# Optimization experiments

Hardware: AMD Instinct MI355X
Metric: run time of the kernel (lower is better)

## Reference

```python
import jax, jax.numpy as jnp
import numpy as np

B, S, H, D = 2, 2048, 16, 128

def setup_inputs() -> dict:
    key = jax.random.key(0)
    kq, kk, kv = jax.random.split(key, 3)
    query = jax.random.normal(kq, (B, S, H, D), dtype=jnp.float32)
    key_t = jax.random.normal(kk, (B, S, H, D), dtype=jnp.float32)
    value = jax.random.normal(kv, (B, S, H, D), dtype=jnp.float32)
    return {"query": query, "key": key_t, "value": value}

def reference(query, key, value):
    # Single-device equivalent: SeqAllToAll4D is identity (world_size=1),
    # ring flash attention == exact softmax attention.
    # Layout [B, S, H, D] (flash-attn convention), non-causal, no dropout.
    scale = 1.0 / jnp.sqrt(jnp.asarray(query.shape[-1], query.dtype))
    # scores: [B, H, Sq, Sk]
    scores = jnp.einsum("bqhd,bkhd->bhqk", query, key) * scale
    probs = jax.nn.softmax(scores, axis=-1)
    out = jnp.einsum("bhqk,bkhd->bqhd", probs, value)
    return out
```

## Files before the change

kernel.cpp:

```cpp
#include <hip/hip_runtime.h>
#include <hip/hip_bf16.h>

#define NB 2
#define NS 2048
#define NH 16
#define ND 128
#define SROW (NH*ND)

#define QBLK 128
#define KBLK 64
#define NTHR 256
#define NT   (NS/KBLK)


typedef __attribute__((ext_vector_type(4))) float f32x4;
typedef __attribute__((ext_vector_type(8))) __bf16 bf16x8;
typedef __attribute__((ext_vector_type(4))) __bf16 bf16x4;
typedef __attribute__((ext_vector_type(8))) short s16x8;
typedef __attribute__((ext_vector_type(4))) short s16x4;

#define AS1(p) ((const __attribute__((address_space(1))) void*)(p))
#define AS3(p) ((__attribute__((address_space(3))) void*)(p))

__device__ __forceinline__ short f2bf(float f) {
  union { float f; unsigned u; } v; v.f = f;
  unsigned r = v.u + 0x7fffu + ((v.u >> 16) & 1u);
  return (short)(r >> 16);
}

__global__ __launch_bounds__(256)
void prep_k2(const float* __restrict__ K, char* __restrict__ Kp) {
  const float sc = 0.08838834764831845f * 1.4426950408889634f;
  size_t i = (size_t)blockIdx.x * 256 + threadIdx.x;
  int g = (int)(i & 31);
  size_t row = i >> 5;
  int h = (int)(row & (NH - 1));
  size_t bs = row >> 4;
  int s = (int)(bs & (NS - 1));
  int b = (int)(bs >> 11);
  float4 x = *(const float4*)(K + row * ND + g * 4);
  bf16x4 w = { (__bf16)(x.x * sc), (__bf16)(x.y * sc), (__bf16)(x.z * sc), (__bf16)(x.w * sc) };
  int bh = b * NH + h;
  int kt = s >> 6, r = s & 63;
  int x8 = r * 256 + g * 8;
  int swz = x8 ^ ((r & 7) << 4);
  *(bf16x4*)(Kp + (((size_t)(bh * 32 + kt)) << 14) + swz) = w;
}

__global__ __launch_bounds__(256)
void prep_v2(const float* __restrict__ V, char* __restrict__ Vp) {
  __shared__ short tile[64 * 136];
  int gid = blockIdx.x;
  int kt = gid & 31;
  int bh = gid >> 5;
  int b = bh >> 4, h = bh & 15;
  int s0 = kt * 64;
  const float* src = V + ((size_t)b * NS * NH + h) * ND;
#pragma unroll
  for (int it = 0; it < 8; ++it) {
    int idx = threadIdx.x + it * 256;
    int r = idx >> 5;
    int c = (idx & 31) * 4;
    float4 x = *(const float4*)(src + (size_t)(s0 + r) * SROW + c);
    bf16x4 w = { (__bf16)x.x, (__bf16)x.y, (__bf16)x.z, (__bf16)x.w };
    *(bf16x4*)&tile[r * 136 + c] = w;
  }
  __syncthreads();
  char* dst = Vp + (((size_t)(bh * 32 + kt)) << 14);
#pragma unroll
  for (int it = 0; it < 8; ++it) {
    int id = threadIdx.x + it * 256;
    int d = id >> 4;
    int c = (id >> 1) & 7;
    int half = id & 1;
    int kvb = c * 8 + half * 4;
    s16x4 w = { tile[(kvb + 0) * 136 + d], tile[(kvb + 1) * 136 + d],
                tile[(kvb + 2) * 136 + d], tile[(kvb + 3) * 136 + d] };
    int vb0 = (c >> 2) * 64 + (((c & 3) * 2) & 3) * 16 + ((c & 3) >> 1) * 8;
    int x = d * 128 + vb0 + half * 16;
    int swz = x ^ ((d & 7) << 4);
    *(s16x4*)(dst + swz) = w;
  }
}

__global__ __launch_bounds__(NTHR, 2)
void attn_fwd13(const float* __restrict__ Q, const char* __restrict__ Kp,
                const char* __restrict__ Vp, float* __restrict__ O)
{
  __shared__ __align__(16) char klds[2 * 16384];
  __shared__ __align__(16) char vlds[2 * 16384];

  const int tid  = threadIdx.x;
  const int wave = tid >> 6;
  const int lane = tid & 63;
  const int g    = lane >> 4;
  const int lr   = lane & 15;

  const int L  = blockIdx.x;
  const int bh = (L & 7) + 8 * ((L >> 3) & 3);
  const int qb = L >> 5;
  const int b  = bh >> 4;
  const int h  = bh & 15;

  const float* Qb = Q + ((size_t)b * NS * NH + h) * ND;
  float*       Ob = O + ((size_t)b * NS * NH + h) * ND;
  const char*  kimg = Kp + ((size_t)bh << 19);
  const char*  vimg = Vp + ((size_t)bh << 19);

  const int wq0 = qb * QBLK + wave * 32;

  bf16x8 qf[2][4];
#pragma unroll
  for (int qt = 0; qt < 2; ++qt) {
    const float* qp = Qb + (size_t)(wq0 + qt * 16 + lr) * SROW;
#pragma unroll
    for (int kc = 0; kc < 4; ++kc) {
      const int d0 = kc * 32 + g * 8;
      float4 a = *(const float4*)(qp + d0);
      float4 c = *(const float4*)(qp + d0 + 4);
      bf16x8 f;
      f[0] = (__bf16)a.x; f[1] = (__bf16)a.y; f[2] = (__bf16)a.z; f[3] = (__bf16)a.w;
      f[4] = (__bf16)c.x; f[5] = (__bf16)c.y; f[6] = (__bf16)c.z; f[7] = (__bf16)c.w;
      qf[qt][kc] = f;
    }
  }

  f32x4 oacc[2][8];
#pragma unroll
  for (int qt = 0; qt < 2; ++qt)
#pragma unroll
    for (int dc = 0; dc < 8; ++dc) oacc[qt][dc] = (f32x4){0.f, 0.f, 0.f, 0.f};
  float lpart[2] = {0.f, 0.f};

  const int kmask = (lr & 7) << 4;
  int kca[4];
#pragma unroll
  for (int kc = 0; kc < 4; ++kc)
    kca[kc] = (lr * 256 + kc * 64 + g * 16) ^ kmask;
  const int vca0 = (lr * 128 + g * 16) ^ kmask;
  const int vca1 = (lr * 128 + 64 + g * 16) ^ kmask;

  const int stago = wave * 4096 + lane * 16;
  const int stagl = wave * 4096;

#define STAGE(PAR, KT)                                                         \
  {                                                                            \
    const char* kg = kimg + ((size_t)(KT) << 14) + stago;                      \
    const char* vg = vimg + ((size_t)(KT) << 14) + stago;                      \
    _Pragma("unroll")                                                          \
    for (int ii = 0; ii < 4; ++ii) {                                           \
      __builtin_amdgcn_global_load_lds(AS1(kg + ii * 1024),                    \
          AS3(klds + (PAR) * 16384 + stagl + ii * 1024), 16, 0, 0);            \
      __builtin_amdgcn_global_load_lds(AS1(vg + ii * 1024),                    \
          AS3(vlds + (PAR) * 16384 + stagl + ii * 1024), 16, 0, 0);            \
    }                                                                          \
  }

  STAGE(0, 0);
  __syncthreads();

#pragma unroll 2
  for (int kt = 0; kt < NT; ++kt) {
    const int po = (kt & 1) * 16384;

    if (kt + 1 < NT) STAGE((kt + 1) & 1, kt + 1);

    f32x4 sacc[2][4];
    __builtin_amdgcn_s_setprio(1);
#pragma unroll
    for (int nb = 0; nb < 4; ++nb) {
      f32x4 a0 = {0.f, 0.f, 0.f, 0.f};
      f32x4 a1 = {0.f, 0.f, 0.f, 0.f};
#pragma unroll
      for (int kc = 0; kc < 4; ++kc) {
        bf16x8 kf = *(const bf16x8*)(klds + po + nb * 4096 + kca[kc]);
        a0 = __builtin_amdgcn_mfma_f32_16x16x32_bf16(kf, qf[0][kc], a0, 0, 0, 0);
        a1 = __builtin_amdgcn_mfma_f32_16x16x32_bf16(kf, qf[1][kc], a1, 0, 0, 0);
      }
      sacc[0][nb] = a0;
      sacc[1][nb] = a1;
    }
    __builtin_amdgcn_s_setprio(0);

    bf16x8 pf[2][2];
#pragma unroll
    for (int qt = 0; qt < 2; ++qt) {
#pragma unroll
      for (int nb = 0; nb < 4; ++nb)
#pragma unroll
        for (int i = 0; i < 4; ++i) {
          float p = exp2f(sacc[qt][nb][i]);
          sacc[qt][nb][i] = p;
          lpart[qt] += p;
        }
      bf16x8 t0, t1;
#pragma unroll
      for (int i = 0; i < 4; ++i) {
        t0[i]     = (__bf16)sacc[qt][0][i];
        t0[i + 4] = (__bf16)sacc[qt][1][i];
        t1[i]     = (__bf16)sacc[qt][2][i];
        t1[i + 4] = (__bf16)sacc[qt][3][i];
      }
      pf[qt][0] = t0;
      pf[qt][1] = t1;
    }

    __builtin_amdgcn_s_setprio(1);
#pragma unroll
    for (int dc = 0; dc < 8; ++dc) {
      bf16x8 vf0 = *(const bf16x8*)(vlds + po + dc * 2048 + vca0);
      bf16x8 vf1 = *(const bf16x8*)(vlds + po + dc * 2048 + vca1);
      oacc[0][dc] = __builtin_amdgcn_mfma_f32_16x16x32_bf16(pf[0][0], vf0, oacc[0][dc], 0, 0, 0);
      oacc[1][dc] = __builtin_amdgcn_mfma_f32_16x16x32_bf16(pf[1][0], vf0, oacc[1][dc], 0, 0, 0);
      oacc[0][dc] = __builtin_amdgcn_mfma_f32_16x16x32_bf16(pf[0][1], vf1, oacc[0][dc], 0, 0, 0);
      oacc[1][dc] = __builtin_amdgcn_mfma_f32_16x16x32_bf16(pf[1][1], vf1, oacc[1][dc], 0, 0, 0);
    }
    __builtin_amdgcn_s_setprio(0);

    __syncthreads();
  }

#pragma unroll
  for (int qt = 0; qt < 2; ++qt) {
    float l = lpart[qt];
    l += __shfl_xor(l, 16);
    l += __shfl_xor(l, 32);
    float inv = 1.0f / l;
#pragma unroll
    for (int i = 0; i < 4; ++i) {
      float invm = __shfl(inv, g * 4 + i);
      float* orow = Ob + (size_t)(wq0 + qt * 16 + g * 4 + i) * SROW;
#pragma unroll
      for (int dc = 0; dc < 8; ++dc)
        orow[dc * 16 + lr] = oacc[qt][dc][i] * invm;
    }
  }
#undef STAGE
}

__global__ __launch_bounds__(256, 2)
void attn_fwd_legacy(const float* __restrict__ Q, const float* __restrict__ K,
                     const float* __restrict__ V, float* __restrict__ O)
{
  __shared__ __align__(16) short k_lds[64 * 136];
  __shared__ __align__(16) short vt_lds[ND * 72];
  __shared__ __align__(16) short p_lds[4 * 16 * 72];

  const int tid = threadIdx.x;
  const int wave = tid >> 6;
  const int lane = tid & 63;
  const int g = lane >> 4;
  const int lr = lane & 15;

  const int nqb = NS / 64;
  const int qb = blockIdx.x % nqb;
  const int bh = blockIdx.x / nqb;
  const int b = bh / NH;
  const int h = bh % NH;

  const float scale = 0.08838834764831845f * 1.4426950408889634f;
  const size_t base = ((size_t)b * NS * NH + h) * ND;
  const float* Qb = Q + base;
  const float* Kbp = K + base;
  const float* Vb = V + base;
  float* Ob = O + base;
  const int q0 = qb * 64 + wave * 16;

  bf16x8 qf[4];
  {
    const float* qp = Qb + (size_t)(q0 + lr) * SROW;
#pragma unroll
    for (int kc = 0; kc < 4; ++kc) {
      const int d0 = kc * 32 + g * 8;
      float4 a = *(const float4*)(qp + d0);
      float4 c = *(const float4*)(qp + d0 + 4);
      s16x8 f;
      f[0] = f2bf(a.x * scale); f[1] = f2bf(a.y * scale);
      f[2] = f2bf(a.z * scale); f[3] = f2bf(a.w * scale);
      f[4] = f2bf(c.x * scale); f[5] = f2bf(c.y * scale);
      f[6] = f2bf(c.z * scale); f[7] = f2bf(c.w * scale);
      qf[kc] = __builtin_bit_cast(bf16x8, f);
    }
  }

  f32x4 oacc[8];
#pragma unroll
  for (int dc = 0; dc < 8; ++dc) oacc[dc] = (f32x4){0.f, 0.f, 0.f, 0.f};
  float mrun[4] = {-1e30f, -1e30f, -1e30f, -1e30f};
  float lrun[4] = {0.f, 0.f, 0.f, 0.f};

  for (int kt = 0; kt < NS / 64; ++kt) {
    const int kv0 = kt * 64;
    __syncthreads();
#pragma unroll
    for (int it = 0; it < 8; ++it) {
      int idx = tid + it * 256;
      int r = idx >> 5;
      int c = (idx & 31) << 2;
      float4 x = *(const float4*)(Kbp + (size_t)(kv0 + r) * SROW + c);
      s16x4 w = { f2bf(x.x), f2bf(x.y), f2bf(x.z), f2bf(x.w) };
      *(s16x4*)&k_lds[r * 136 + c] = w;
    }
#pragma unroll
    for (int it = 0; it < 2; ++it) {
      int sub = tid + it * 256;
      int skv = (sub >> 5) << 2;
      int sd = (sub & 31) << 2;
      const float* vp = Vb + (size_t)(kv0 + skv) * SROW + sd;
      float4 r0 = *(const float4*)(vp);
      float4 r1 = *(const float4*)(vp + SROW);
      float4 r2 = *(const float4*)(vp + 2 * SROW);
      float4 r3 = *(const float4*)(vp + 3 * SROW);
      s16x4 w0 = { f2bf(r0.x), f2bf(r1.x), f2bf(r2.x), f2bf(r3.x) };
      s16x4 w1 = { f2bf(r0.y), f2bf(r1.y), f2bf(r2.y), f2bf(r3.y) };
      s16x4 w2 = { f2bf(r0.z), f2bf(r1.z), f2bf(r2.z), f2bf(r3.z) };
      s16x4 w3 = { f2bf(r0.w), f2bf(r1.w), f2bf(r2.w), f2bf(r3.w) };
      *(s16x4*)&vt_lds[(sd + 0) * 72 + skv] = w0;
      *(s16x4*)&vt_lds[(sd + 1) * 72 + skv] = w1;
      *(s16x4*)&vt_lds[(sd + 2) * 72 + skv] = w2;
      *(s16x4*)&vt_lds[(sd + 3) * 72 + skv] = w3;
    }
    __syncthreads();

    f32x4 sacc[4];
#pragma unroll
    for (int nb = 0; nb < 4; ++nb) {
      f32x4 acc = {0.f, 0.f, 0.f, 0.f};
#pragma unroll
      for (int kc = 0; kc < 4; ++kc) {
        bf16x8 kfr = *(const bf16x8*)&k_lds[(nb * 16 + lr) * 136 + kc * 32 + g * 8];
        acc = __builtin_amdgcn_mfma_f32_16x16x32_bf16(qf[kc], kfr, acc, 0, 0, 0);
      }
      sacc[nb] = acc;
    }

    float alpha[4];
#pragma unroll
    for (int i = 0; i < 4; ++i) {
      float m = fmaxf(fmaxf(sacc[0][i], sacc[1][i]), fmaxf(sacc[2][i], sacc[3][i]));
#pragma unroll
      for (int off = 1; off < 16; off <<= 1) m = fmaxf(m, __shfl_xor(m, off));
      float mnew = fmaxf(mrun[i], m);
      alpha[i] = exp2f(mrun[i] - mnew);
      mrun[i] = mnew;
    }
    float rsum[4] = {0.f, 0.f, 0.f, 0.f};
#pragma unroll
    for (int nb = 0; nb < 4; ++nb)
#pragma unroll
      for (int i = 0; i < 4; ++i) {
        float p = exp2f(sacc[nb][i] - mrun[i]);
        sacc[nb][i] = p;
        rsum[i] += p;
      }
#pragma unroll
    for (int i = 0; i < 4; ++i) {
#pragma unroll
      for (int off = 1; off < 16; off <<= 1) rsum[i] += __shfl_xor(rsum[i], off);
      lrun[i] = lrun[i] * alpha[i] + rsum[i];
    }
#pragma unroll
    for (int dc = 0; dc < 8; ++dc)
#pragma unroll
      for (int i = 0; i < 4; ++i) oacc[dc][i] *= alpha[i];

    short* pw = &p_lds[wave * 16 * 72];
#pragma unroll
    for (int nb = 0; nb < 4; ++nb)
#pragma unroll
      for (int i = 0; i < 4; ++i)
        pw[(g * 4 + i) * 72 + nb * 16 + lr] = f2bf(sacc[nb][i]);

    bf16x8 pf0 = *(const bf16x8*)&pw[lr * 72 + g * 8];
    bf16x8 pf1 = *(const bf16x8*)&pw[lr * 72 + 32 + g * 8];

#pragma unroll
    for (int dc = 0; dc < 8; ++dc) {
      bf16x8 vf0 = *(const bf16x8*)&vt_lds[(dc * 16 + lr) * 72 + g * 8];
      oacc[dc] = __builtin_amdgcn_mfma_f32_16x16x32_bf16(pf0, vf0, oacc[dc], 0, 0, 0);
      bf16x8 vf1 = *(const bf16x8*)&vt_lds[(dc * 16 + lr) * 72 + 32 + g * 8];
      oacc[dc] = __builtin_amdgcn_mfma_f32_16x16x32_bf16(pf1, vf1, oacc[dc], 0, 0, 0);
    }
  }

  float* op = Ob + (size_t)q0 * SROW;
#pragma unroll
  for (int i = 0; i < 4; ++i) {
    float inv = 1.0f / lrun[i];
    int m = g * 4 + i;
#pragma unroll
    for (int dc = 0; dc < 8; ++dc)
      op[(size_t)m * SROW + dc * 16 + lr] = oacc[dc][i] * inv;
  }
}

extern "C" void kernel_launch(void* const* d_in, const int* in_sizes, int n_in,
                              void* d_out, int out_size, void* d_ws, size_t ws_size,
                              hipStream_t stream) {
  const float* Q = (const float*)d_in[0];
  const float* K = (const float*)d_in[1];
  const float* V = (const float*)d_in[2];
  float* O = (float*)d_out;

  const size_t elems = (size_t)NB * NS * NH * ND;
  const size_t need = 2 * elems * sizeof(short);

  if (ws_size >= need) {
    char* Kp = (char*)d_ws;
    char* Vp = Kp + elems * sizeof(short);
    hipLaunchKernelGGL(prep_k2, dim3((unsigned)(elems / 4 / 256)), dim3(256), 0, stream, K, Kp);
    hipLaunchKernelGGL(prep_v2, dim3(32 * 32), dim3(256), 0, stream, V, Vp);
    hipLaunchKernelGGL(attn_fwd13, dim3(NB * NH * (NS / QBLK)), dim3(NTHR), 0, stream,
                       Q, Kp, Vp, O);
  } else {
    hipLaunchKernelGGL(attn_fwd_legacy, dim3(NB * NH * (NS / 64)), dim3(256), 0, stream, Q, K, V, O);
  }
}
```

Before: 101.2 us.

## Software-pipeline QK and PV across iterations with triple-buffered V tiles

```diff
diff --git a/kernel.cpp b/kernel.cpp
--- a/kernel.cpp
+++ b/kernel.cpp
@@ -84,11 +84,11 @@
 }
 
 __global__ __launch_bounds__(NTHR, 2)
-void attn_fwd13(const float* __restrict__ Q, const char* __restrict__ Kp,
+void attn_fwd14(const float* __restrict__ Q, const char* __restrict__ Kp,
                 const char* __restrict__ Vp, float* __restrict__ O)
 {
   __shared__ __align__(16) char klds[2 * 16384];
-  __shared__ __align__(16) char vlds[2 * 16384];
+  __shared__ __align__(16) char vlds[3 * 16384];
 
   const int tid  = threadIdx.x;
   const int wave = tid >> 6;
@@ -143,81 +143,110 @@
   const int stago = wave * 4096 + lane * 16;
   const int stagl = wave * 4096;
 
-#define STAGE(PAR, KT)                                                         \
+#define STAGE(KT)                                                              \
   {                                                                            \
+    const int kpar_ = ((KT) & 1) * 16384;                                      \
+    const int vpar_ = ((KT) % 3) * 16384;                                      \
     const char* kg = kimg + ((size_t)(KT) << 14) + stago;                      \
     const char* vg = vimg + ((size_t)(KT) << 14) + stago;                      \
     _Pragma("unroll")                                                          \
     for (int ii = 0; ii < 4; ++ii) {                                           \
       __builtin_amdgcn_global_load_lds(AS1(kg + ii * 1024),                    \
-          AS3(klds + (PAR) * 16384 + stagl + ii * 1024), 16, 0, 0);            \
+          AS3(klds + kpar_ + stagl + ii * 1024), 16, 0, 0);                    \
       __builtin_amdgcn_global_load_lds(AS1(vg + ii * 1024),                    \
-          AS3(vlds + (PAR) * 16384 + stagl + ii * 1024), 16, 0, 0);            \
+          AS3(vlds + vpar_ + stagl + ii * 1024), 16, 0, 0);                    \
     }                                                                          \
   }
 
-  STAGE(0, 0);
+#define QK(KT, SC)                                                             \
+  {                                                                            \
+    const int po_ = ((KT) & 1) * 16384;                                        \
+    __builtin_amdgcn_s_setprio(1);                                             \
+    _Pragma("unroll")                                                          \
+    for (int nb = 0; nb < 4; ++nb) {                                           \
+      f32x4 a0 = {0.f, 0.f, 0.f, 0.f};                                         \
+      f32x4 a1 = {0.f, 0.f, 0.f, 0.f};                                         \
+      _Pragma("unroll")                                                        \
+      for (int kc = 0; kc < 4; ++kc) {                                         \
+        bf16x8 kf = *(const bf16x8*)(klds + po_ + nb * 4096 + kca[kc]);        \
+        a0 = __builtin_amdgcn_mfma_f32_16x16x32_bf16(kf, qf[0][kc], a0, 0, 0, 0); \
+        a1 = __builtin_amdgcn_mfma_f32_16x16x32_bf16(kf, qf[1][kc], a1, 0, 0, 0); \
+      }                                                                        \
+      SC[0][nb] = a0;                                                          \
+      SC[1][nb] = a1;                                                          \
+    }                                                                          \
+    __builtin_amdgcn_s_setprio(0);                                             \
+  }
+
+#define SM(SP, PF)                                                             \
+  {                                                                            \
+    _Pragma("unroll")                                                          \
+    for (int qt = 0; qt < 2; ++qt) {                                           \
+      _Pragma("unroll")                                                        \
+      for (int nb = 0; nb < 4; ++nb)                                           \
+        _Pragma("unroll")                                                      \
+        for (int i = 0; i < 4; ++i) {                                          \
+          float p = exp2f(SP[qt][nb][i]);                                      \
+          SP[qt][nb][i] = p;                                                   \
+          lpart[qt] += p;                                                      \
+        }                                                                      \
+      bf16x8 t0, t1;                                                           \
+      _Pragma("unroll")                                                        \
+      for (int i = 0; i < 4; ++i) {                                            \
+        t0[i]     = (__bf16)SP[qt][0][i];                                      \
+        t0[i + 4] = (__bf16)SP[qt][1][i];                                      \
+        t1[i]     = (__bf16)SP[qt][2][i];                                      \
+        t1[i + 4] = (__bf16)SP[qt][3][i];                                      \
+      }                                                                        \
+      PF[qt][0] = t0;                                                          \
+      PF[qt][1] = t1;                                                          \
+    }                                                                          \
+  }
+
+#define PV(KT, PF)                                                             \
+  {                                                                            \
+    const int po_ = ((KT) % 3) * 16384;                                        \
+    __builtin_amdgcn_s_setprio(1);                                             \
+    _Pragma("unroll")                                                          \
+    for (int dc = 0; dc < 8; ++dc) {                                           \
+      bf16x8 vf0 = *(const bf16x8*)(vlds + po_ + dc * 2048 + vca0);            \
+      bf16x8 vf1 = *(const bf16x8*)(vlds + po_ + dc * 2048 + vca1);            \
+      oacc[0][dc] = __builtin_amdgcn_mfma_f32_16x16x32_bf16(PF[0][0], vf0, oacc[0][dc], 0, 0, 0); \
+      oacc[1][dc] = __builtin_amdgcn_mfma_f32_16x16x32_bf16(PF[1][0], vf0, oacc[1][dc], 0, 0, 0); \
+      oacc[0][dc] = __builtin_amdgcn_mfma_f32_16x16x32_bf16(PF[0][1], vf1, oacc[0][dc], 0, 0, 0); \
+      oacc[1][dc] = __builtin_amdgcn_mfma_f32_16x16x32_bf16(PF[1][1], vf1, oacc[1][dc], 0, 0, 0); \
+    }                                                                          \
+    __builtin_amdgcn_s_setprio(0);                                             \
+  }
+
+#define BODY(KT, SP, SC)                                                       \
+  {                                                                            \
+    if ((KT) + 1 < NT) STAGE((KT) + 1);                                        \
+    QK(KT, SC);                                                                \
+    bf16x8 pf[2][2];                                                           \
+    SM(SP, pf);                                                                \
+    PV((KT) - 1, pf);                                                          \
+    __syncthreads();                                                           \
+  }
+
+  f32x4 sA[2][4], sB[2][4];
+
+  STAGE(0);
   __syncthreads();
-
-#pragma unroll 2
-  for (int kt = 0; kt < NT; ++kt) {
-    const int po = (kt & 1) * 16384;
-
-    if (kt + 1 < NT) STAGE((kt + 1) & 1, kt + 1);
-
-    f32x4 sacc[2][4];
-    __builtin_amdgcn_s_setprio(1);
-#pragma unroll
-    for (int nb = 0; nb < 4; ++nb) {
-      f32x4 a0 = {0.f, 0.f, 0.f, 0.f};
-      f32x4 a1 = {0.f, 0.f, 0.f, 0.f};
-#pragma unroll
-      for (int kc = 0; kc < 4; ++kc) {
-        bf16x8 kf = *(const bf16x8*)(klds + po + nb * 4096 + kca[kc]);
-        a0 = __builtin_amdgcn_mfma_f32_16x16x32_bf16(kf, qf[0][kc], a0, 0, 0, 0);
-        a1 = __builtin_amdgcn_mfma_f32_16x16x32_bf16(kf, qf[1][kc], a1, 0, 0, 0);
-      }
-      sacc[0][nb] = a0;
-      sacc[1][nb] = a1;
-    }
-    __builtin_amdgcn_s_setprio(0);
-
+  STAGE(1);
+  QK(0, sA);
+  __syncthreads();
+
+  for (int kt = 1; kt + 1 < NT; kt += 2) {
+    BODY(kt, sA, sB);
+    BODY(kt + 1, sB, sA);
+  }
+  BODY(NT - 1, sA, sB);
+
+  {
     bf16x8 pf[2][2];
-#pragma unroll
-    for (int qt = 0; qt < 2; ++qt) {
-#pragma unroll
-      for (int nb = 0; nb < 4; ++nb)
-#pragma unroll
-        for (int i = 0; i < 4; ++i) {
-          float p = exp2f(sacc[qt][nb][i]);
-          sacc[qt][nb][i] = p;
-          lpart[qt] += p;
-        }
-      bf16x8 t0, t1;
-#pragma unroll
-      for (int i = 0; i < 4; ++i) {
-        t0[i]     = (__bf16)sacc[qt][0][i];
-        t0[i + 4] = (__bf16)sacc[qt][1][i];
-        t1[i]     = (__bf16)sacc[qt][2][i];
-        t1[i + 4] = (__bf16)sacc[qt][3][i];
-      }
-      pf[qt][0] = t0;
-      pf[qt][1] = t1;
-    }
-
-    __builtin_amdgcn_s_setprio(1);
-#pragma unroll
-    for (int dc = 0; dc < 8; ++dc) {
-      bf16x8 vf0 = *(const bf16x8*)(vlds + po + dc * 2048 + vca0);
-      bf16x8 vf1 = *(const bf16x8*)(vlds + po + dc * 2048 + vca1);
-      oacc[0][dc] = __builtin_amdgcn_mfma_f32_16x16x32_bf16(pf[0][0], vf0, oacc[0][dc], 0, 0, 0);
-      oacc[1][dc] = __builtin_amdgcn_mfma_f32_16x16x32_bf16(pf[1][0], vf0, oacc[1][dc], 0, 0, 0);
-      oacc[0][dc] = __builtin_amdgcn_mfma_f32_16x16x32_bf16(pf[0][1], vf1, oacc[0][dc], 0, 0, 0);
-      oacc[1][dc] = __builtin_amdgcn_mfma_f32_16x16x32_bf16(pf[1][1], vf1, oacc[1][dc], 0, 0, 0);
-    }
-    __builtin_amdgcn_s_setprio(0);
-
-    __syncthreads();
+    SM(sB, pf);
+    PV(NT - 1, pf);
   }
 
 #pragma unroll
@@ -236,6 +265,10 @@
     }
   }
 #undef STAGE
+#undef QK
+#undef SM
+#undef PV
+#undef BODY
 }
 
 __global__ __launch_bounds__(256, 2)
@@ -410,7 +443,7 @@
     char* Vp = Kp + elems * sizeof(short);
     hipLaunchKernelGGL(prep_k2, dim3((unsigned)(elems / 4 / 256)), dim3(256), 0, stream, K, Kp);
     hipLaunchKernelGGL(prep_v2, dim3(32 * 32), dim3(256), 0, stream, V, Vp);
-    hipLaunchKernelGGL(attn_fwd13, dim3(NB * NH * (NS / QBLK)), dim3(NTHR), 0, stream,
+    hipLaunchKernelGGL(attn_fwd14, dim3(NB * NH * (NS / QBLK)), dim3(NTHR), 0, stream,
                        Q, Kp, Vp, O);
   } else {
     hipLaunchKernelGGL(attn_fwd_legacy, dim3(NB * NH * (NS / 64)), dim3(256), 0, stream, Q, K, V, O);
```

After: 104.5 us. 1.03x slower.
